# Kernel optimization log

Measured on AMD Instinct MI355X. Metric: run time of the kernel, lower is better.

## Reference

```python
import jax, jax.numpy as jnp
import numpy as np

B_SZ, NSPLIT, OUT, IN = 2048, 256, 256, 256  # in == out == nsplit required by the bias broadcast in the original layer


def setup_inputs() -> dict:
    key = jax.random.key(0)
    kx, ka, kb = jax.random.split(key, 3)
    x = jax.random.normal(kx, (B_SZ, NSPLIT, IN), dtype=jnp.float32)
    A = jax.random.normal(ka, (1, NSPLIT, OUT, IN), dtype=jnp.float32) * 0.02
    Bp = jax.random.normal(kb, (1, OUT, IN), dtype=jnp.float32) * 0.02
    return {"x": x, "A": A, "Bp": Bp}


def reference(x, A, Bp):
    # Original TF: reduce_sum(expand_dims(x, -2) * A, axis=3) + B
    # == per-group (nsplit) dense transform: y[b,n,o] = sum_i x[b,n,i] * A[0,n,o,i]
    # Expressed as a batched GEMM via einsum (no (b,n,o,i) intermediate).
    y = jnp.einsum('bni,noi->bno', x, A[0])  # (B, nsplit, out)
    # Bias add broadcasts (1, out, in) against (B, nsplit, out); valid since nsplit == out == in.
    return y + Bp
```

## Files before the change

kernel.cpp:

```cpp
#include <hip/hip_runtime.h>


#define B_SZ   2048
#define NS     256
#define OUTD   256
#define IND    256

#define MT     64
#define BK     32
#define LDK    40

typedef __bf16 bf16x8 __attribute__((ext_vector_type(8)));
typedef __bf16 bf16x4 __attribute__((ext_vector_type(4)));
typedef float  floatx4 __attribute__((ext_vector_type(4)));

__device__ inline bf16x4 cvt4(floatx4 v) {
    bf16x4 r;
    r[0] = (__bf16)v[0];
    r[1] = (__bf16)v[1];
    r[2] = (__bf16)v[2];
    r[3] = (__bf16)v[3];
    return r;
}

__global__ __launch_bounds__(256, 3)
void md_kernel(const float* __restrict__ x,
               const float* __restrict__ A,
               const float* __restrict__ Bp,
               float* __restrict__ out) {
    __shared__ __bf16 Xs[MT * LDK];
    __shared__ __bf16 As[OUTD * LDK];
    __shared__ float  bias_s[OUTD];

    const int bid  = blockIdx.x;
    const int batch = (bid & 7) * 32 + (bid >> 8);
    const int mtile = (bid >> 3) & 31;
    const int m0    = mtile * MT;

    const int t    = threadIdx.x;
    const int wid  = t >> 6;
    const int lane = t & 63;
    const int l15  = lane & 15;
    const int lq   = lane >> 4;

    bias_s[t] = Bp[batch * OUTD + t];

    const float* xg = x + (size_t)m0 * (NS * IND) + (size_t)batch * IND;
    const float* Ag = A + (size_t)batch * OUTD * IND;

    floatx4 acc[4][4];
#pragma unroll
    for (int i = 0; i < 4; ++i)
#pragma unroll
        for (int j = 0; j < 4; ++j)
            acc[i][j] = (floatx4){0.f, 0.f, 0.f, 0.f};

    const int r_lo = t >> 3;
    const int k4   = (t & 7) * 4;

#pragma unroll 1
    for (int kt = 0; kt < IND / BK; ++kt) {
        const int kbase = kt * BK;
#pragma unroll
        for (int j = 0; j < 2; ++j) {
            const int row = j * 32 + r_lo;
            floatx4 v = *(const floatx4*)(xg + (size_t)row * (NS * IND) + kbase + k4);
            *(bf16x4*)(&Xs[row * LDK + k4]) = cvt4(v);
        }
#pragma unroll
        for (int j = 0; j < 8; ++j) {
            const int row = j * 32 + r_lo;
            floatx4 v = *(const floatx4*)(Ag + (size_t)row * IND + kbase + k4);
            *(bf16x4*)(&As[row * LDK + k4]) = cvt4(v);
        }
        __syncthreads();

        bf16x8 a_frag[4], b_frag[4];
#pragma unroll
        for (int i = 0; i < 4; ++i)
            a_frag[i] = *(const bf16x8*)(&Xs[(i * 16 + l15) * LDK + lq * 8]);
#pragma unroll
        for (int j = 0; j < 4; ++j)
            b_frag[j] = *(const bf16x8*)(&As[(wid * 64 + j * 16 + l15) * LDK + lq * 8]);

#pragma unroll
        for (int i = 0; i < 4; ++i)
#pragma unroll
            for (int j = 0; j < 4; ++j)
                acc[i][j] = __builtin_amdgcn_mfma_f32_16x16x32_bf16(
                    a_frag[i], b_frag[j], acc[i][j], 0, 0, 0);

        __syncthreads();
    }

    float* og = out + (size_t)m0 * (NS * OUTD) + (size_t)batch * OUTD;
#pragma unroll
    for (int i = 0; i < 4; ++i) {
#pragma unroll
        for (int j = 0; j < 4; ++j) {
            const int o = wid * 64 + j * 16 + l15;
            const float b = bias_s[o];
#pragma unroll
            for (int r = 0; r < 4; ++r) {
                const int bm = i * 16 + lq * 4 + r;
                og[(size_t)bm * (NS * OUTD) + o] = acc[i][j][r] + b;
            }
        }
    }
}

extern "C" void kernel_launch(void* const* d_in, const int* in_sizes, int n_in,
                              void* d_out, int out_size, void* d_ws, size_t ws_size,
                              hipStream_t stream) {
    const float* x  = (const float*)d_in[0];
    const float* A  = (const float*)d_in[1];
    const float* Bp = (const float*)d_in[2];
    float* out = (float*)d_out;

    dim3 grid((B_SZ / MT) * NS);
    dim3 block(256);
    hipLaunchKernelGGL(md_kernel, grid, block, 0, stream, x, A, Bp, out);
}
```

Measured before the change: 1.027 ms.

## Keep full per-group A in LDS, stream x directly into registers per wave

Replaces the 64-row tile grid with one 1024-thread block per group n. Each block converts that group's entire A matrix to bf16 once into about 128KB of LDS, laid out in MFMA fragment order. Each wave then streams x rows from global memory straight into registers, with a two-deep prefetch. This removes the repeated A reloads and the per-k-step LDS barriers. The trade-off is that only 256 blocks run, each needing a very large LDS allocation (one block per CU), and there is no LDS staging for x, which may reduce occupancy and latency hiding.

```diff
diff --git a/kernel.cpp b/kernel.cpp
--- a/kernel.cpp
+++ b/kernel.cpp
@@ -1,112 +1,99 @@
 #include <hip/hip_runtime.h>
 
 
-#define B_SZ   2048
 #define NS     256
 #define OUTD   256
 #define IND    256
-
-#define MT     64
-#define BK     32
-#define LDK    40
+#define ROWF   65536
 
 typedef __bf16 bf16x8 __attribute__((ext_vector_type(8)));
-typedef __bf16 bf16x4 __attribute__((ext_vector_type(4)));
 typedef float  floatx4 __attribute__((ext_vector_type(4)));
 
-__device__ inline bf16x4 cvt4(floatx4 v) {
-    bf16x4 r;
-    r[0] = (__bf16)v[0];
-    r[1] = (__bf16)v[1];
-    r[2] = (__bf16)v[2];
-    r[3] = (__bf16)v[3];
-    return r;
-}
-
-__global__ __launch_bounds__(256, 3)
+__global__ __launch_bounds__(1024, 4)
 void md_kernel(const float* __restrict__ x,
                const float* __restrict__ A,
                const float* __restrict__ Bp,
                float* __restrict__ out) {
-    __shared__ __bf16 Xs[MT * LDK];
-    __shared__ __bf16 As[OUTD * LDK];
-    __shared__ float  bias_s[OUTD];
+    extern __shared__ char smem[];
+    __bf16* As     = (__bf16*)smem;
+    float*  bias_s = (float*)(smem + 131072);
 
-    const int bid  = blockIdx.x;
-    const int batch = (bid & 7) * 32 + (bid >> 8);
-    const int mtile = (bid >> 3) & 31;
-    const int m0    = mtile * MT;
-
+    const int n    = blockIdx.x;
     const int t    = threadIdx.x;
-    const int wid  = t >> 6;
+    const int w    = t >> 6;
     const int lane = t & 63;
     const int l15  = lane & 15;
     const int lq   = lane >> 4;
 
-    bias_s[t] = Bp[batch * OUTD + t];
+    {
+        const float* Ag = A + (size_t)n * (OUTD * IND);
+#pragma unroll
+        for (int it = 0; it < 8; ++it) {
+            const int e  = it * 1024 + t;
+            const int o  = (((e >> 6) & 15) << 4) | (e & 15);
+            const int k0 = ((e >> 10) << 5) | (((e >> 4) & 3) << 3);
+            const float* src = Ag + o * IND + k0;
+            const floatx4 p0 = *(const floatx4*)src;
+            const floatx4 p1 = *(const floatx4*)(src + 4);
+            bf16x8 v;
+            v[0]=(__bf16)p0[0]; v[1]=(__bf16)p0[1]; v[2]=(__bf16)p0[2]; v[3]=(__bf16)p0[3];
+            v[4]=(__bf16)p1[0]; v[5]=(__bf16)p1[1]; v[6]=(__bf16)p1[2]; v[7]=(__bf16)p1[3];
+            *(bf16x8*)(As + (size_t)e * 8) = v;
+        }
+        if (t < OUTD) bias_s[t] = Bp[n * OUTD + t];
+    }
+    __syncthreads();
 
-    const float* xg = x + (size_t)m0 * (NS * IND) + (size_t)batch * IND;
-    const float* Ag = A + (size_t)batch * OUTD * IND;
+    const float* xw = x + (size_t)(w * 128 + l15) * ROWF + n * IND + lq * 8;
+    float*       ow = out + (size_t)(w * 128) * ROWF + n * OUTD;
 
-    floatx4 acc[4][4];
+    floatx4 acc[16];
 #pragma unroll
-    for (int i = 0; i < 4; ++i)
-#pragma unroll
-        for (int j = 0; j < 4; ++j)
-            acc[i][j] = (floatx4){0.f, 0.f, 0.f, 0.f};
+    for (int j = 0; j < 16; ++j) acc[j] = (floatx4){0.f, 0.f, 0.f, 0.f};
 
-    const int r_lo = t >> 3;
-    const int k4   = (t & 7) * 4;
+#define XADDR(q) (xw + (size_t)((q) >> 3) * (16 * ROWF) + ((q) & 7) * 32)
+
+    floatx4 s0a = *(const floatx4*)XADDR(0);
+    floatx4 s0b = *(const floatx4*)(XADDR(0) + 4);
+    floatx4 s1a = *(const floatx4*)XADDR(1);
+    floatx4 s1b = *(const floatx4*)(XADDR(1) + 4);
+
+#define BODY(q, sa, sb)                                                          \
+    {                                                                            \
+        bf16x8 a;                                                                \
+        a[0]=(__bf16)sa[0]; a[1]=(__bf16)sa[1]; a[2]=(__bf16)sa[2]; a[3]=(__bf16)sa[3]; \
+        a[4]=(__bf16)sb[0]; a[5]=(__bf16)sb[1]; a[6]=(__bf16)sb[2]; a[7]=(__bf16)sb[3]; \
+        if ((q) < 62) {                                                          \
+            sa = *(const floatx4*)XADDR((q) + 2);                                \
+            sb = *(const floatx4*)(XADDR((q) + 2) + 4);                          \
+        }                                                                        \
+        const __bf16* bp = As + ((q) & 7) * 8192 + lane * 8;                     \
+        _Pragma("unroll")                                                        \
+        for (int j = 0; j < 16; ++j) {                                           \
+            const bf16x8 b = *(const bf16x8*)(bp + j * 512);                     \
+            acc[j] = __builtin_amdgcn_mfma_f32_16x16x32_bf16(a, b, acc[j], 0, 0, 0); \
+        }                                                                        \
+        if (((q) & 7) == 7) {                           \
+            float* og = ow + (size_t)((q) >> 3) * (16 * ROWF);                   \
+            _Pragma("unroll")                                                    \
+            for (int j = 0; j < 16; ++j) {                                       \
+                const float bb = bias_s[j * 16 + l15];                           \
+                _Pragma("unroll")                                                \
+                for (int r = 0; r < 4; ++r)                                      \
+                    og[(size_t)(lq * 4 + r) * ROWF + j * 16 + l15] = acc[j][r] + bb; \
+                acc[j] = (floatx4){0.f, 0.f, 0.f, 0.f};                          \
+            }                                                                    \
+        }                                                                        \
+    }
 
 #pragma unroll 1
-    for (int kt = 0; kt < IND / BK; ++kt) {
-        const int kbase = kt * BK;
-#pragma unroll
-        for (int j = 0; j < 2; ++j) {
-            const int row = j * 32 + r_lo;
-            floatx4 v = *(const floatx4*)(xg + (size_t)row * (NS * IND) + kbase + k4);
-            *(bf16x4*)(&Xs[row * LDK + k4]) = cvt4(v);
-        }
-#pragma unroll
-        for (int j = 0; j < 8; ++j) {
-            const int row = j * 32 + r_lo;
-            floatx4 v = *(const floatx4*)(Ag + (size_t)row * IND + kbase + k4);
-            *(bf16x4*)(&As[row * LDK + k4]) = cvt4(v);
-        }
-        __syncthreads();
-
-        bf16x8 a_frag[4], b_frag[4];
-#pragma unroll
-        for (int i = 0; i < 4; ++i)
-            a_frag[i] = *(const bf16x8*)(&Xs[(i * 16 + l15) * LDK + lq * 8]);
-#pragma unroll
-        for (int j = 0; j < 4; ++j)
-            b_frag[j] = *(const bf16x8*)(&As[(wid * 64 + j * 16 + l15) * LDK + lq * 8]);
-
-#pragma unroll
-        for (int i = 0; i < 4; ++i)
-#pragma unroll
-            for (int j = 0; j < 4; ++j)
-                acc[i][j] = __builtin_amdgcn_mfma_f32_16x16x32_bf16(
-                    a_frag[i], b_frag[j], acc[i][j], 0, 0, 0);
-
-        __syncthreads();
+    for (int qq = 0; qq < 32; ++qq) {
+        const int q0 = qq * 2;
+        BODY(q0,     s0a, s0b);
+        BODY(q0 + 1, s1a, s1b);
     }
-
-    float* og = out + (size_t)m0 * (NS * OUTD) + (size_t)batch * OUTD;
-#pragma unroll
-    for (int i = 0; i < 4; ++i) {
-#pragma unroll
-        for (int j = 0; j < 4; ++j) {
-            const int o = wid * 64 + j * 16 + l15;
-            const float b = bias_s[o];
-#pragma unroll
-            for (int r = 0; r < 4; ++r) {
-                const int bm = i * 16 + lq * 4 + r;
-                og[(size_t)bm * (NS * OUTD) + o] = acc[i][j][r] + b;
-            }
-        }
-    }
+#undef BODY
+#undef XADDR
 }
 
 extern "C" void kernel_launch(void* const* d_in, const int* in_sizes, int n_in,
@@ -117,7 +104,13 @@
     const float* Bp = (const float*)d_in[2];
     float* out = (float*)d_out;
 
-    dim3 grid((B_SZ / MT) * NS);
-    dim3 block(256);
-    hipLaunchKernelGGL(md_kernel, grid, block, 0, stream, x, A, Bp, out);
+    static bool attr_done = false;
+    if (!attr_done) {
+        hipFuncSetAttribute((const void*)md_kernel,
+                            hipFuncAttributeMaxDynamicSharedMemorySize, 132096);
+        attr_done = true;
+    }
+
+    hipLaunchKernelGGL(md_kernel, dim3(NS), dim3(1024), 132096, stream,
+                       x, A, Bp, out);
 }
```

After: 918.1 us. 10.6% less time.
